# Kernel tuning notes

Hardware: AMD Instinct MI355X
Metric: run time of the kernel (lower is better)

## Reference

```python
import jax, jax.numpy as jnp
import numpy as np

B, S, K_IN = 8, 2048, 128
D_MODEL, N_INPUT, N_PROC = 1024, 256, 1024
K_PROC = 256


def setup_inputs() -> dict:
    key = jax.random.key(0)
    k1, k2, k3, k4 = jax.random.split(key, 4)
    selected_input_acts = jax.random.normal(k1, (B, S, K_IN), dtype=jnp.float32)
    input_idx = jax.random.randint(k2, (B, K_IN), 0, N_INPUT)
    # learned params (orthogonal init in torch; random normal is fine for a numeric baseline)
    process_weights = jax.random.normal(k3, (N_PROC, N_INPUT), dtype=jnp.float32) * (2.0 / N_INPUT) ** 0.5
    process_outputs = jax.random.normal(k4, (N_PROC, D_MODEL), dtype=jnp.float32) * (2.0 / N_PROC) ** 0.5
    return {
        "selected_input_acts": selected_input_acts,
        "process_weights": process_weights,
        "process_outputs": process_outputs,
        "input_idx": input_idx,
        "k_process": K_PROC,
    }


def reference(selected_input_acts, process_weights, process_outputs, input_idx, k_process):
    # gather per-batch columns of process_weights: [B, k_input, n_process]
    sel_w = process_weights.T[input_idx]  # (N,P) indexed by (B,k) -> (B,k,P)
    # bmm + exact (erf) gelu, matching torch F.gelu default: [B, S, n_process]
    process_acts = jax.nn.gelu(
        jnp.einsum("bsk,bkp->bsp", selected_input_acts, sel_w),
        approximate=False,
    )
    # router: mean over sequence, top-k process neurons per batch
    process_scores = process_acts.mean(axis=1)  # [B, n_process]
    _, process_idx = jax.lax.top_k(process_scores, k_process)  # [B, k_process]
    # gather selected activations: [B, S, k_process]
    sel_acts = jnp.take_along_axis(process_acts, process_idx[:, None, :], axis=2)
    # gather selected output vectors: [B, k_process, d_model]
    sel_out = process_outputs[process_idx]
    # combine: [B, S, d_model]
    output = jnp.einsum("bsk,bkd->bsd", sel_acts, sel_out)
    return output
```

## Files before the change

kernel.cpp:

```cpp
#include <hip/hip_runtime.h>
#include <hip/hip_bf16.h>

#define NB    8
#define NS    2048
#define NKIN  128
#define NPROC 1024
#define NIN   256
#define NDM   1024
#define NKP   256
#define NSEG  32

typedef unsigned short u16;
typedef unsigned int   u32;
typedef __attribute__((ext_vector_type(4))) u16   u16x4;
typedef __attribute__((ext_vector_type(8))) u16   u16x8;
typedef __attribute__((ext_vector_type(4))) float f32x4;
typedef __attribute__((ext_vector_type(8))) short bf16x8;
typedef __attribute__((ext_vector_type(4))) float f32x4v;

__device__ __forceinline__ float bf2f(u16 u) {
    union { u32 i; float f; } v; v.i = ((u32)u) << 16; return v.f;
}
__device__ __forceinline__ u16 f2bf(float f) {
    u32 x = __float_as_uint(f);
    u32 r = (x + 0x7FFFu + ((x >> 16) & 1u)) >> 16;
    return (u16)r;
}
__device__ __forceinline__ float gelu_fast(float x) {
    float y  = fabsf(x) * 0.70710678118654752f;
    float t  = __builtin_amdgcn_rcpf(fmaf(0.3275911f, y, 1.0f));
    float p  = t * fmaf(t, fmaf(t, fmaf(t, fmaf(t, 1.061405429f,
               -1.453152027f), 1.421413741f), -0.284496736f), 0.254829592f);
    float e  = __expf(-y * y);
    float er = fmaf(-p, e, 1.0f);
    float s  = copysignf(er, x);
    return 0.5f * x * (1.0f + s);
}
__device__ __forceinline__ int clampi(int v, int hi) {
    return v < 0 ? 0 : (v > hi ? hi : v);
}

__global__ __launch_bounds__(256) void k0_merged(
        const float* __restrict__ A, const float* __restrict__ W,
        const int* __restrict__ idx, u16* __restrict__ AHi,
        u16* __restrict__ ALo, u16* __restrict__ WgHi,
        u16* __restrict__ WgLo) {
    const int blk = blockIdx.x;
    const int tid = threadIdx.x;
    if (blk < 1024) {
        size_t i = ((size_t)blk * 256 + tid) * 8;
        f32x4 a = *(const f32x4*)&A[i];
        f32x4 c = *(const f32x4*)&A[i + 4];
        u16x8 h, l;
        #pragma unroll
        for (int j = 0; j < 4; ++j) {
            u16 hj = f2bf(a[j]); h[j] = hj;     l[j]     = f2bf(a[j] - bf2f(hj));
            u16 hk = f2bf(c[j]); h[j + 4] = hk; l[j + 4] = f2bf(c[j] - bf2f(hk));
        }
        *(u16x8*)&AHi[i] = h;
        *(u16x8*)&ALo[i] = l;
    } else {
        const int q  = blk - 1024;
        const int b  = q >> 3;
        const int p0 = (q & 7) * 128;
        __shared__ int idxs[NKIN];
        if (tid < NKIN) idxs[tid] = clampi(idx[b * NKIN + tid], NIN - 1);
        __syncthreads();
        for (int e = tid; e < 128 * NKIN; e += 256) {
            int p = p0 + (e >> 7), k = e & 127;
            float x  = W[p * NIN + idxs[k]];
            u16 hi   = f2bf(x);
            u16 lo   = f2bf(x - bf2f(hi));
            size_t o = (size_t)(b * NPROC + p) * NKIN + k;
            WgHi[o] = hi;
            WgLo[o] = lo;
        }
    }
}

__global__ __launch_bounds__(256) void k1_scores(
        const u16* __restrict__ AHi, const u16* __restrict__ ALo,
        const u16* __restrict__ WgHi, const u16* __restrict__ WgLo,
        float* __restrict__ scores, u16* __restrict__ acts) {
    const int lin  = blockIdx.x;
    const int b    = lin & 7;
    const int q    = lin >> 3;
    const int pblk = q & 15;
    const int sblk = q >> 4;
    const int p0 = pblk * 64, s0 = sblk * 64;
    const int tid  = threadIdx.x;
    const int lane = tid & 63;
    const int wid  = tid >> 6;
    const int wr   = wid >> 1;
    const int wc   = wid & 1;
    const int lr   = lane & 15;
    const int kr   = lane >> 4;

    __shared__ u16  pool[4 * 64 * 40];
    __shared__ float red[2][64];
    char* const pb = (char*)pool;

    f32x4v acc[2][2] = {};

    for (int kc = 0; kc < 4; ++kc) {
        __syncthreads();
        {
            int r = tid >> 2, g = tid & 3;
            size_t src = (size_t)(b * NS + s0 + r) * NKIN + kc * 32 + g * 8;
            u32 off = (u32)r * 80 + (u32)g * 16;
            *(u16x8*)(pb + off)         = *(const u16x8*)&AHi[src];
            *(u16x8*)(pb + 5120 + off)  = *(const u16x8*)&ALo[src];
        }
        {
            int pp = tid >> 2, g = tid & 3;
            size_t src = (size_t)(b * NPROC + p0 + pp) * NKIN + kc * 32 + g * 8;
            u32 off = (u32)pp * 80 + (u32)g * 16;
            *(u16x8*)(pb + 10240 + off) = *(const u16x8*)&WgHi[src];
            *(u16x8*)(pb + 15360 + off) = *(const u16x8*)&WgLo[src];
        }
        __syncthreads();

        const u32 kb = (u32)kr * 16;
        bf16x8 ah[2], al[2], wh[2], wl[2];
        #pragma unroll
        for (int m = 0; m < 2; ++m) {
            u32 row = (u32)(wr * 32 + m * 16 + lr);
            u32 off = row * 80 + kb;
            ah[m] = *(const bf16x8*)(pb + off);
            al[m] = *(const bf16x8*)(pb + 5120 + off);
        }
        #pragma unroll
        for (int n = 0; n < 2; ++n) {
            u32 col = (u32)(wc * 32 + n * 16 + lr);
            u32 off = col * 80 + kb;
            wh[n] = *(const bf16x8*)(pb + 10240 + off);
            wl[n] = *(const bf16x8*)(pb + 15360 + off);
        }
        #pragma unroll
        for (int m = 0; m < 2; ++m)
            #pragma unroll
            for (int n = 0; n < 2; ++n) {
                acc[m][n] = __builtin_amdgcn_mfma_f32_16x16x32_bf16(
                    ah[m], wh[n], acc[m][n], 0, 0, 0);
                acc[m][n] = __builtin_amdgcn_mfma_f32_16x16x32_bf16(
                    ah[m], wl[n], acc[m][n], 0, 0, 0);
                acc[m][n] = __builtin_amdgcn_mfma_f32_16x16x32_bf16(
                    al[m], wh[n], acc[m][n], 0, 0, 0);
            }
    }

    __syncthreads();
    float colsum[2] = {0.f, 0.f};
    #pragma unroll
    for (int n = 0; n < 2; ++n)
        #pragma unroll
        for (int m = 0; m < 2; ++m)
            #pragma unroll
            for (int j = 0; j < 4; ++j) {
                float g = gelu_fast(acc[m][n][j]);
                colsum[n] += g;
                if (acts) {
                    u32 row = (u32)(wr * 32 + m * 16 + kr * 4 + j);
                    u32 col = (u32)(wc * 32 + n * 16 + lr);
                    *(u16*)(pb + row * 128 + col * 2) = f2bf(g);
                }
            }
    #pragma unroll
    for (int n = 0; n < 2; ++n) {
        colsum[n] += __shfl_xor(colsum[n], 16, 64);
        colsum[n] += __shfl_xor(colsum[n], 32, 64);
    }
    if (lane < 16) {
        #pragma unroll
        for (int n = 0; n < 2; ++n)
            red[wr][wc * 32 + n * 16 + lane] = colsum[n];
    }
    __syncthreads();
    if (tid < 64)
        scores[(size_t)(sblk * NB + b) * NPROC + p0 + tid] =
            red[0][tid] + red[1][tid];
    if (acts) {
        #pragma unroll
        for (int e = tid; e < 512; e += 256) {
            int row = e >> 3, g = e & 7;
            *(u16x8*)&acts[(size_t)(b * NS + s0 + row) * NPROC + p0 + g * 8] =
                *(const u16x8*)(pb + (u32)row * 128 + (u32)g * 16);
        }
    }
}

__global__ __launch_bounds__(256) void k2_topk(
        const float* __restrict__ scores, int* __restrict__ topk) {
    const int b  = blockIdx.x;
    const int pc = blockIdx.y;
    __shared__ float sc[NPROC];
    #pragma unroll
    for (int q = 0; q < 4; ++q) {
        int p = q * 256 + threadIdx.x;
        float v = 0.f;
        #pragma unroll
        for (int seg = 0; seg < NSEG; ++seg)
            v += scores[(size_t)(seg * NB + b) * NPROC + p];
        sc[p] = v;
    }
    __syncthreads();
    const int p = pc * 256 + threadIdx.x;
    const float v = sc[p];
    int rank = 0;
    #pragma unroll 4
    for (int jj = 0; jj < NPROC / 4; ++jj) {
        f32x4 s4 = *(const f32x4*)&sc[jj * 4];
        #pragma unroll
        for (int c = 0; c < 4; ++c) {
            int j = jj * 4 + c;
            rank += (s4[c] > v) || (s4[c] == v && j < p);
        }
    }
    if (rank < NKP) topk[b * NKP + rank] = p;
}

__global__ __launch_bounds__(256) void k3_gather(
        const u16* __restrict__ acts, const int* __restrict__ topk,
        u16* __restrict__ sel) {
    const int lin   = blockIdx.x;
    const int b     = lin & 7;
    const int q     = lin >> 3;
    const int chalf = q & 1;
    const int sblk  = q >> 1;
    const int c0 = chalf * 128, s0 = sblk * 64;
    const int tid = threadIdx.x;

    __shared__ int tcol[128];
    if (tid < 128) tcol[tid] = clampi(topk[b * NKP + c0 + tid], NPROC - 1);
    __syncthreads();

    const int c     = tid & 127;
    const int rhalf = tid >> 7;
    const int src_c = tcol[c];
    #pragma unroll 8
    for (int r = 0; r < 32; ++r) {
        int row = s0 + rhalf * 32 + r;
        sel[(size_t)(b * NS + row) * NKP + c0 + c] =
            acts[(size_t)(b * NS + row) * NPROC + src_c];
    }
}

__global__ __launch_bounds__(256) void k3_selacts(
        const u16* __restrict__ AHi, const u16* __restrict__ WgHi,
        const int* __restrict__ topk, u16* __restrict__ sel) {
    const int lin  = blockIdx.x;
    const int b    = lin & 7;
    const int q    = lin >> 3;
    const int cblk = q & 3;
    const int sblk = q >> 2;
    const int c0g = cblk * 64, s0 = sblk * 64;
    const int tid  = threadIdx.x;
    const int lane = tid & 63;
    const int wid  = tid >> 6;
    const int wr   = wid >> 1;
    const int wc   = wid & 1;
    const int lr   = lane & 15;
    const int kr   = lane >> 4;

    __shared__ int tcol[64];
    if (tid < 64) tcol[tid] = clampi(topk[b * NKP + c0g + tid], NPROC - 1);
    __syncthreads();

    const u16* ap[2];
    const u16* wp[2];
    #pragma unroll
    for (int m = 0; m < 2; ++m)
        ap[m] = &AHi[(size_t)(b * NS + s0 + wr * 32 + m * 16 + lr) * NKIN + kr * 8];
    #pragma unroll
    for (int n = 0; n < 2; ++n)
        wp[n] = &WgHi[(size_t)(b * NPROC + tcol[wc * 32 + n * 16 + lr]) * NKIN + kr * 8];

    bf16x8 af[2][4], bf[2][4];
    #pragma unroll
    for (int ks = 0; ks < 4; ++ks) {
        #pragma unroll
        for (int m = 0; m < 2; ++m) af[m][ks] = *(const bf16x8*)(ap[m] + ks * 32);
        #pragma unroll
        for (int n = 0; n < 2; ++n) bf[n][ks] = *(const bf16x8*)(wp[n] + ks * 32);
    }

    f32x4v acc[2][2] = {};
    #pragma unroll
    for (int ks = 0; ks < 4; ++ks)
        #pragma unroll
        for (int m = 0; m < 2; ++m)
            #pragma unroll
            for (int n = 0; n < 2; ++n)
                acc[m][n] = __builtin_amdgcn_mfma_f32_16x16x32_bf16(
                    af[m][ks], bf[n][ks], acc[m][n], 0, 0, 0);

    #pragma unroll
    for (int m = 0; m < 2; ++m) {
        const int rbase = s0 + wr * 32 + m * 16 + (lane >> 4) * 4;
        #pragma unroll
        for (int n = 0; n < 2; ++n) {
            const int col = c0g + wc * 32 + n * 16 + lr;
            #pragma unroll
            for (int j = 0; j < 4; ++j)
                sel[(size_t)(b * NS + rbase + j) * NKP + col] =
                    f2bf(gelu_fast(acc[m][n][j]));
        }
    }
}

__global__ __launch_bounds__(256) void k4_mfma(
        const u16* __restrict__ sel, const float* __restrict__ PO,
        const int* __restrict__ topk, float* __restrict__ out) {
    const int lin  = blockIdx.x;
    const int b    = lin & 7;
    const int q    = lin >> 3;
    const int dblk = q & 7;
    const int sblk = q >> 3;
    const int d0 = dblk * 128, s0 = sblk * 128;
    const int tid  = threadIdx.x;
    const int lane = tid & 63;
    const int wid  = tid >> 6;
    const int wr   = wid >> 1;
    const int wc   = wid & 1;

    __shared__ int tloc[NKP];
    __shared__ u16 Alds[128 * 64];
    __shared__ u16 Blds[128 * 64];

    tloc[tid] = clampi(topk[b * NKP + tid], NPROC - 1);

    f32x4v acc[4][4] = {};

    for (int k0 = 0; k0 < NKP; k0 += 64) {
        __syncthreads();
        for (int e = tid; e < 1024; e += 256) {
            int r = e >> 3, g = e & 7;
            u16x8 v = *(const u16x8*)&sel[(size_t)(b * NS + s0 + r) * NKP + k0 + g * 8];
            int slot = g ^ (r & 7);
            *(u16x8*)&Alds[r * 64 + slot * 8] = v;
        }
        for (int e = tid; e < 1024; e += 256) {
            int kp = e >> 5, cg = e & 31;
            f32x4 p0v = *(const f32x4*)&PO[(size_t)tloc[k0 + kp * 2]     * NDM + d0 + cg * 4];
            f32x4 p1v = *(const f32x4*)&PO[(size_t)tloc[k0 + kp * 2 + 1] * NDM + d0 + cg * 4];
            #pragma unroll
            for (int j = 0; j < 4; ++j) {
                int n = cg * 4 + j;
                u32 pack = (u32)f2bf(p0v[j]) | ((u32)f2bf(p1v[j]) << 16);
                u32 byteoff = (u32)n * 128 + (((u32)kp * 4) ^ (((u32)n & 7) << 4));
                *(u32*)((char*)Blds + byteoff) = pack;
            }
        }
        __syncthreads();

        #pragma unroll
        for (int kk = 0; kk < 2; ++kk) {
            const u32 kbase2 = (u32)(kk * 64 + (lane >> 4) * 16);
            bf16x8 afrag[4], bfrag[4];
            #pragma unroll
            for (int m = 0; m < 4; ++m) {
                u32 row = (u32)(wr * 64 + m * 16 + (lane & 15));
                u32 byteoff = row * 128 + (kbase2 ^ ((row & 7) << 4));
                afrag[m] = *(const bf16x8*)((const char*)Alds + byteoff);
            }
            #pragma unroll
            for (int n = 0; n < 4; ++n) {
                u32 col = (u32)(wc * 64 + n * 16 + (lane & 15));
                u32 byteoff = col * 128 + (kbase2 ^ ((col & 7) << 4));
                bfrag[n] = *(const bf16x8*)((const char*)Blds + byteoff);
            }
            #pragma unroll
            for (int m = 0; m < 4; ++m)
                #pragma unroll
                for (int n = 0; n < 4; ++n)
                    acc[m][n] = __builtin_amdgcn_mfma_f32_16x16x32_bf16(
                        afrag[m], bfrag[n], acc[m][n], 0, 0, 0);
        }
    }

    #pragma unroll
    for (int m = 0; m < 4; ++m) {
        const int rbase = s0 + wr * 64 + m * 16 + (lane >> 4) * 4;
        #pragma unroll
        for (int n = 0; n < 4; ++n) {
            const int col = d0 + wc * 64 + n * 16 + (lane & 15);
            #pragma unroll
            for (int j = 0; j < 4; ++j)
                out[(size_t)(b * NS + rbase + j) * NDM + col] = acc[m][n][j];
        }
    }
}

extern "C" void kernel_launch(void* const* d_in, const int* in_sizes, int n_in,
                              void* d_out, int out_size, void* d_ws, size_t ws_size,
                              hipStream_t stream) {
    (void)in_sizes; (void)n_in; (void)out_size;
    const float* A   = (const float*)d_in[0];
    const float* W   = (const float*)d_in[1];
    const float* PO  = (const float*)d_in[2];
    const int*   idx = (const int*)d_in[3];
    float* out = (float*)d_out;

    char* w = (char*)d_ws;
    u16*   sel    = (u16*)w;
    float* scores = (float*)(w + (size_t)8388608);
    int*   topk   = (int*)(w + (size_t)9437184);
    u16*   WgHi   = (u16*)(w + (size_t)9445376);
    u16*   WgLo   = (u16*)(w + (size_t)11542528);
    u16*   AHi    = (u16*)(w + (size_t)13639680);
    u16*   ALo    = (u16*)(w + (size_t)17833984);
    u16*   acts   = (u16*)(w + (size_t)22028288);
    const bool big = ws_size >= (size_t)22028288 + 33554432;

    k0_merged<<<1024 + 64, 256, 0, stream>>>(A, W, idx, AHi, ALo, WgHi, WgLo);
    k1_scores<<<4096, 256, 0, stream>>>(AHi, ALo, WgHi, WgLo, scores,
                                        big ? acts : (u16*)nullptr);
    k2_topk<<<dim3(NB, 4), 256, 0, stream>>>(scores, topk);
    if (big)
        k3_gather<<<512, 256, 0, stream>>>(acts, topk, sel);
    else
        k3_selacts<<<1024, 256, 0, stream>>>(AHi, WgHi, topk, sel);
    k4_mfma<<<1024, 256, 0, stream>>>(sel, PO, topk, out);
}
```

Measured before the change: 113.9 us.

## Store activations transposed and fuse top-k gather into output GEMM

k1 now writes GELU activations in a process-major (transposed) layout through an XOR-swizzled LDS staging tile. The separate gather kernel is removed, and a new fused kernel loads the selected activation rows directly by topk index, along with the matching process_outputs rows. It then runs the bf16 MFMA GEMM to produce the output. This drops the intermediate sel buffer round trip and one kernel launch. In exchange the fused kernel does scalar LDS transposes inside its load loop and reloads PO rows per d-block.

```diff
diff --git a/kernel.cpp b/kernel.cpp
--- a/kernel.cpp
+++ b/kernel.cpp
@@ -81,7 +81,7 @@
 __global__ __launch_bounds__(256) void k1_scores(
         const u16* __restrict__ AHi, const u16* __restrict__ ALo,
         const u16* __restrict__ WgHi, const u16* __restrict__ WgLo,
-        float* __restrict__ scores, u16* __restrict__ acts) {
+        float* __restrict__ scores, u16* __restrict__ acts_t) {
     const int lin  = blockIdx.x;
     const int b    = lin & 7;
     const int q    = lin >> 3;
@@ -159,10 +159,12 @@
             for (int j = 0; j < 4; ++j) {
                 float g = gelu_fast(acc[m][n][j]);
                 colsum[n] += g;
-                if (acts) {
-                    u32 row = (u32)(wr * 32 + m * 16 + kr * 4 + j);
-                    u32 col = (u32)(wc * 32 + n * 16 + lr);
-                    *(u16*)(pb + row * 128 + col * 2) = f2bf(g);
+                if (acts_t) {
+                    u32 p = (u32)(wc * 32 + n * 16 + lr);
+                    u32 s = (u32)(wr * 32 + m * 16 + kr * 4 + j);
+                    u32 off = p * 128 + ((((s >> 3) ^ (p & 7)) & 7) << 4)
+                              + (s & 7) * 2;
+                    *(u16*)(pb + off) = f2bf(g);
                 }
             }
     #pragma unroll
@@ -179,12 +181,13 @@
     if (tid < 64)
         scores[(size_t)(sblk * NB + b) * NPROC + p0 + tid] =
             red[0][tid] + red[1][tid];
-    if (acts) {
+    if (acts_t) {
         #pragma unroll
         for (int e = tid; e < 512; e += 256) {
-            int row = e >> 3, g = e & 7;
-            *(u16x8*)&acts[(size_t)(b * NS + s0 + row) * NPROC + p0 + g * 8] =
-                *(const u16x8*)(pb + (u32)row * 128 + (u32)g * 16);
+            int r = e >> 3, g = e & 7;
+            u32 off = (u32)r * 128 + ((((u32)g ^ ((u32)r & 7)) & 7) << 4);
+            *(u16x8*)&acts_t[(size_t)(b * NPROC + p0 + r) * NS + s0 + g * 8] =
+                *(const u16x8*)(pb + off);
         }
     }
 }
@@ -219,29 +222,95 @@
     if (rank < NKP) topk[b * NKP + rank] = p;
 }
 
-__global__ __launch_bounds__(256) void k3_gather(
-        const u16* __restrict__ acts, const int* __restrict__ topk,
-        u16* __restrict__ sel) {
-    const int lin   = blockIdx.x;
-    const int b     = lin & 7;
-    const int q     = lin >> 3;
-    const int chalf = q & 1;
-    const int sblk  = q >> 1;
-    const int c0 = chalf * 128, s0 = sblk * 64;
-    const int tid = threadIdx.x;
-
-    __shared__ int tcol[128];
-    if (tid < 128) tcol[tid] = clampi(topk[b * NKP + c0 + tid], NPROC - 1);
-    __syncthreads();
-
-    const int c     = tid & 127;
-    const int rhalf = tid >> 7;
-    const int src_c = tcol[c];
-    #pragma unroll 8
-    for (int r = 0; r < 32; ++r) {
-        int row = s0 + rhalf * 32 + r;
-        sel[(size_t)(b * NS + row) * NKP + c0 + c] =
-            acts[(size_t)(b * NS + row) * NPROC + src_c];
+__global__ __launch_bounds__(256) void k4_fused(
+        const u16* __restrict__ acts_t, const float* __restrict__ PO,
+        const int* __restrict__ topk, float* __restrict__ out) {
+    const int lin  = blockIdx.x;
+    const int b    = lin & 7;
+    const int q    = lin >> 3;
+    const int dblk = q & 7;
+    const int sblk = q >> 3;
+    const int d0 = dblk * 128, s0 = sblk * 128;
+    const int tid  = threadIdx.x;
+    const int lane = tid & 63;
+    const int wid  = tid >> 6;
+    const int wr   = wid >> 1;
+    const int wc   = wid & 1;
+
+    __shared__ int tloc[NKP];
+    __shared__ u16 Alds[128 * 64];
+    __shared__ u16 Blds[128 * 64];
+
+    tloc[tid] = clampi(topk[b * NKP + tid], NPROC - 1);
+
+    f32x4v acc[4][4] = {};
+
+    for (int k0 = 0; k0 < NKP; k0 += 64) {
+        __syncthreads();
+        for (int e = tid; e < 1024; e += 256) {
+            int r = e >> 4, g = e & 15;
+            u16x8 v = *(const u16x8*)&acts_t[
+                (size_t)(b * NPROC + tloc[k0 + r]) * NS + s0 + g * 8];
+            #pragma unroll
+            for (int j = 0; j < 8; ++j) {
+                u32 s = (u32)(g * 8 + j);
+                u32 sw = (s & 7) ^ ((s >> 3) & 7);
+                u32 off = s * 128 + (((((u32)r >> 3) ^ sw) & 7) << 4)
+                          + ((u32)r & 7) * 2;
+                *(u16*)((char*)Alds + off) = v[j];
+            }
+        }
+        for (int e = tid; e < 1024; e += 256) {
+            int kp = e >> 5, cg = e & 31;
+            f32x4 p0v = *(const f32x4*)&PO[(size_t)tloc[k0 + kp * 2]     * NDM + d0 + cg * 4];
+            f32x4 p1v = *(const f32x4*)&PO[(size_t)tloc[k0 + kp * 2 + 1] * NDM + d0 + cg * 4];
+            #pragma unroll
+            for (int j = 0; j < 4; ++j) {
+                int n = cg * 4 + j;
+                u32 pack = (u32)f2bf(p0v[j]) | ((u32)f2bf(p1v[j]) << 16);
+                u32 byteoff = (u32)n * 128 + (((u32)kp * 4) ^ (((u32)n & 7) << 4));
+                *(u32*)((char*)Blds + byteoff) = pack;
+            }
+        }
+        __syncthreads();
+
+        #pragma unroll
+        for (int kk = 0; kk < 2; ++kk) {
+            const u32 slotk  = (u32)(kk * 4 + (lane >> 4));
+            const u32 kbase2 = (u32)(kk * 64 + (lane >> 4) * 16);
+            bf16x8 afrag[4], bfrag[4];
+            #pragma unroll
+            for (int m = 0; m < 4; ++m) {
+                u32 row = (u32)(wr * 64 + m * 16 + (lane & 15));
+                u32 sw  = (row & 7) ^ ((row >> 3) & 7);
+                u32 byteoff = row * 128 + (((slotk ^ sw) & 7) << 4);
+                afrag[m] = *(const bf16x8*)((const char*)Alds + byteoff);
+            }
+            #pragma unroll
+            for (int n = 0; n < 4; ++n) {
+                u32 col = (u32)(wc * 64 + n * 16 + (lane & 15));
+                u32 byteoff = col * 128 + (kbase2 ^ ((col & 7) << 4));
+                bfrag[n] = *(const bf16x8*)((const char*)Blds + byteoff);
+            }
+            #pragma unroll
+            for (int m = 0; m < 4; ++m)
+                #pragma unroll
+                for (int n = 0; n < 4; ++n)
+                    acc[m][n] = __builtin_amdgcn_mfma_f32_16x16x32_bf16(
+                        afrag[m], bfrag[n], acc[m][n], 0, 0, 0);
+        }
+    }
+
+    #pragma unroll
+    for (int m = 0; m < 4; ++m) {
+        const int rbase = s0 + wr * 64 + m * 16 + (lane >> 4) * 4;
+        #pragma unroll
+        for (int n = 0; n < 4; ++n) {
+            const int col = d0 + wc * 64 + n * 16 + (lane & 15);
+            #pragma unroll
+            for (int j = 0; j < 4; ++j)
+                out[(size_t)(b * NS + rbase + j) * NDM + col] = acc[m][n][j];
+        }
     }
 }
 
@@ -409,16 +478,17 @@
     u16*   WgLo   = (u16*)(w + (size_t)11542528);
     u16*   AHi    = (u16*)(w + (size_t)13639680);
     u16*   ALo    = (u16*)(w + (size_t)17833984);
-    u16*   acts   = (u16*)(w + (size_t)22028288);
+    u16*   acts_t = (u16*)(w + (size_t)22028288);
     const bool big = ws_size >= (size_t)22028288 + 33554432;
 
     k0_merged<<<1024 + 64, 256, 0, stream>>>(A, W, idx, AHi, ALo, WgHi, WgLo);
     k1_scores<<<4096, 256, 0, stream>>>(AHi, ALo, WgHi, WgLo, scores,
-                                        big ? acts : (u16*)nullptr);
+                                        big ? acts_t : (u16*)nullptr);
     k2_topk<<<dim3(NB, 4), 256, 0, stream>>>(scores, topk);
-    if (big)
-        k3_gather<<<512, 256, 0, stream>>>(acts, topk, sel);
-    else
+    if (big) {
+        k4_fused<<<1024, 256, 0, stream>>>(acts_t, PO, topk, out);
+    } else {
         k3_selacts<<<1024, 256, 0, stream>>>(AHi, WgHi, topk, sel);
-    k4_mfma<<<1024, 256, 0, stream>>>(sel, PO, topk, out);
-}
+        k4_mfma<<<1024, 256, 0, stream>>>(sel, PO, topk, out);
+    }
+}
```

Measured after the change: 109.1 us (median of 2 runs). 1.04x faster.

## Store GELU activations transposed and gather selected columns via LDS transpose

Applied to the files above, without the earlier changes.

k1 now writes the activation matrix in [B, P, S] layout, using an XOR-swizzled shared-memory staging buffer, instead of [B, S, P]. The gather kernel is replaced by a transpose kernel. It reads whole contiguous 16-byte rows for each selected neuron, transposes them through swizzled LDS, and writes vectorized [B, S, K] output. The aim is to replace the strided 2-byte scattered gather reads with coalesced vector loads, at the cost of an extra LDS round trip and scalar LDS reads during the transpose.

```diff
diff --git a/kernel.cpp b/kernel.cpp
--- a/kernel.cpp
+++ b/kernel.cpp
@@ -81,7 +81,7 @@
 __global__ __launch_bounds__(256) void k1_scores(
         const u16* __restrict__ AHi, const u16* __restrict__ ALo,
         const u16* __restrict__ WgHi, const u16* __restrict__ WgLo,
-        float* __restrict__ scores, u16* __restrict__ acts) {
+        float* __restrict__ scores, u16* __restrict__ acts_t) {
     const int lin  = blockIdx.x;
     const int b    = lin & 7;
     const int q    = lin >> 3;
@@ -159,10 +159,12 @@
             for (int j = 0; j < 4; ++j) {
                 float g = gelu_fast(acc[m][n][j]);
                 colsum[n] += g;
-                if (acts) {
-                    u32 row = (u32)(wr * 32 + m * 16 + kr * 4 + j);
-                    u32 col = (u32)(wc * 32 + n * 16 + lr);
-                    *(u16*)(pb + row * 128 + col * 2) = f2bf(g);
+                if (acts_t) {
+                    u32 p = (u32)(wc * 32 + n * 16 + lr);
+                    u32 s = (u32)(wr * 32 + m * 16 + kr * 4 + j);
+                    u32 off = p * 128 + ((((s >> 3) ^ (p & 7)) & 7) << 4)
+                              + (s & 7) * 2;
+                    *(u16*)(pb + off) = f2bf(g);
                 }
             }
     #pragma unroll
@@ -179,12 +181,13 @@
     if (tid < 64)
         scores[(size_t)(sblk * NB + b) * NPROC + p0 + tid] =
             red[0][tid] + red[1][tid];
-    if (acts) {
+    if (acts_t) {
         #pragma unroll
         for (int e = tid; e < 512; e += 256) {
-            int row = e >> 3, g = e & 7;
-            *(u16x8*)&acts[(size_t)(b * NS + s0 + row) * NPROC + p0 + g * 8] =
-                *(const u16x8*)(pb + (u32)row * 128 + (u32)g * 16);
+            int r = e >> 3, g = e & 7;
+            u32 off = (u32)r * 128 + ((((u32)g ^ ((u32)r & 7)) & 7) << 4);
+            *(u16x8*)&acts_t[(size_t)(b * NPROC + p0 + r) * NS + s0 + g * 8] =
+                *(const u16x8*)(pb + off);
         }
     }
 }
@@ -219,29 +222,47 @@
     if (rank < NKP) topk[b * NKP + rank] = p;
 }
 
-__global__ __launch_bounds__(256) void k3_gather(
-        const u16* __restrict__ acts, const int* __restrict__ topk,
+__global__ __launch_bounds__(256) void k3t_transpose(
+        const u16* __restrict__ acts_t, const int* __restrict__ topk,
         u16* __restrict__ sel) {
-    const int lin   = blockIdx.x;
-    const int b     = lin & 7;
-    const int q     = lin >> 3;
-    const int chalf = q & 1;
-    const int sblk  = q >> 1;
-    const int c0 = chalf * 128, s0 = sblk * 64;
+    const int lin = blockIdx.x;
+    const int b   = lin & 7;
+    const int q   = lin >> 3;
+    const int ct  = q & 3;
+    const int st  = q >> 2;
+    const int c0 = ct * 64, s0 = st * 64;
     const int tid = threadIdx.x;
 
-    __shared__ int tcol[128];
-    if (tid < 128) tcol[tid] = clampi(topk[b * NKP + c0 + tid], NPROC - 1);
-    __syncthreads();
-
-    const int c     = tid & 127;
-    const int rhalf = tid >> 7;
-    const int src_c = tcol[c];
-    #pragma unroll 8
-    for (int r = 0; r < 32; ++r) {
-        int row = s0 + rhalf * 32 + r;
-        sel[(size_t)(b * NS + row) * NKP + c0 + c] =
-            acts[(size_t)(b * NS + row) * NPROC + src_c];
+    __shared__ int tcol[64];
+    __shared__ u16 Tl[64 * 64];
+
+    if (tid < 64) tcol[tid] = clampi(topk[b * NKP + c0 + tid], NPROC - 1);
+    __syncthreads();
+
+    #pragma unroll
+    for (int it = 0; it < 2; ++it) {
+        int e = tid + it * 256;
+        int c = e >> 3, sg = e & 7;
+        u16x8 v = *(const u16x8*)&acts_t[
+            (size_t)(b * NPROC + tcol[c]) * NS + s0 + sg * 8];
+        u32 off = (u32)c * 128 + (((u32)sg ^ ((u32)c & 7)) << 4);
+        *(u16x8*)((char*)Tl + off) = v;
+    }
+    __syncthreads();
+
+    #pragma unroll
+    for (int it = 0; it < 2; ++it) {
+        int s  = ((tid >> 3) & 7) * 8 + (tid >> 6) + it * 4;
+        int cg = tid & 7;
+        u16x8 v;
+        #pragma unroll
+        for (int i = 0; i < 8; ++i) {
+            u32 c = (u32)(cg * 8 + i);
+            u32 off = c * 128 + (((((u32)s >> 3) ^ (c & 7)) & 7) << 4)
+                      + ((u32)s & 7) * 2;
+            v[i] = *(const u16*)((const char*)Tl + off);
+        }
+        *(u16x8*)&sel[(size_t)(b * NS + s0 + s) * NKP + c0 + cg * 8] = v;
     }
 }
 
@@ -409,16 +430,17 @@
     u16*   WgLo   = (u16*)(w + (size_t)11542528);
     u16*   AHi    = (u16*)(w + (size_t)13639680);
     u16*   ALo    = (u16*)(w + (size_t)17833984);
-    u16*   acts   = (u16*)(w + (size_t)22028288);
+    u16*   acts_t = (u16*)(w + (size_t)22028288);
     const bool big = ws_size >= (size_t)22028288 + 33554432;
 
     k0_merged<<<1024 + 64, 256, 0, stream>>>(A, W, idx, AHi, ALo, WgHi, WgLo);
     k1_scores<<<4096, 256, 0, stream>>>(AHi, ALo, WgHi, WgLo, scores,
-                                        big ? acts : (u16*)nullptr);
+                                        big ? acts_t : (u16*)nullptr);
     k2_topk<<<dim3(NB, 4), 256, 0, stream>>>(scores, topk);
-    if (big)
-        k3_gather<<<512, 256, 0, stream>>>(acts, topk, sel);
-    else
+    if (big) {
+        k3t_transpose<<<1024, 256, 0, stream>>>(acts_t, topk, sel);
+    } else {
         k3_selacts<<<1024, 256, 0, stream>>>(AHi, WgHi, topk, sel);
+    }
     k4_mfma<<<1024, 256, 0, stream>>>(sel, PO, topk, out);
 }
```

Result: faster. 111.3 us (-2.2%).
